# Performance work log

Measured on AMD Instinct MI355X. Metric: run time of the kernel, lower is better.

Reference implementation:

```python
import jax, jax.numpy as jnp
import numpy as np

B, S, E = 4, 2048, 1024
H = 16
D = E // H  # head_dim = 64


def setup_inputs() -> dict:
    key = jax.random.key(0)
    ks = jax.random.split(key, 7)
    query = jax.random.normal(ks[0], (B, S, E), dtype=jnp.float32)
    k_in = jax.random.normal(ks[1], (B, S, E), dtype=jnp.float32)
    v_in = jax.random.normal(ks[2], (B, S, E), dtype=jnp.float32)
    lim_qkv = 1.0 / np.sqrt(E)
    W_qkv = jax.random.uniform(ks[3], (E, 3 * E), jnp.float32, -lim_qkv, lim_qkv)
    b_qkv = jax.random.uniform(ks[4], (3 * E,), jnp.float32, -lim_qkv, lim_qkv)
    W_out = jax.random.uniform(ks[5], (E, E), jnp.float32, -lim_qkv, lim_qkv)
    b_out = jax.random.uniform(ks[6], (E,), jnp.float32, -lim_qkv, lim_qkv)
    return {"query": query, "key": k_in, "value": v_in,
            "W_qkv": W_qkv, "b_qkv": b_qkv, "W_out": W_out, "b_out": b_out}


def reference(query, key, value, W_qkv, b_qkv, W_out, b_out):
    # NOTE: original module ignores key/value; q,k,v all derived from query.
    b, s, e = query.shape
    qkv = query @ W_qkv + b_qkv                     # [B,S,3E]
    qkv = qkv.reshape(b, s, 3, H, D)
    q, k, v = qkv[:, :, 0], qkv[:, :, 1], qkv[:, :, 2]   # [B,S,H,D]
    scale = jnp.sqrt(jnp.asarray(D, dtype=jnp.float32))
    scores = jnp.einsum('bqhd,bkhd->bhqk', q, k) / scale  # [B,H,S,S]
    attn = jax.nn.softmax(scores, axis=-1)
    out = jnp.einsum('bhqk,bkhd->bqhd', attn, v).reshape(b, s, e)
    return out @ W_out + b_out
```

## Files before the change

kernel.cpp:

```cpp
#include <hip/hip_runtime.h>
#include <hip/hip_bf16.h>

#define Bc 4
#define Sc 2048
#define Ec 1024
#define Hc 16
#define Dc 64

typedef __bf16 bf16_t;
typedef __bf16 bf16x8 __attribute__((ext_vector_type(8)));
typedef float f32x4 __attribute__((ext_vector_type(4)));

extern "C" __device__ float __ocml_native_exp2_f32(float);

__device__ __forceinline__ f32x4 mfma16(bf16x8 a, bf16x8 b, f32x4 c) {
    return __builtin_amdgcn_mfma_f32_16x16x32_bf16(a, b, c, 0, 0, 0);
}

__device__ __forceinline__ void gload16(const bf16_t* g, bf16_t* l) {
    __builtin_amdgcn_global_load_lds(
        (const __attribute__((address_space(1))) unsigned int*)g,
        (__attribute__((address_space(3))) unsigned int*)l, 16, 0, 0);
}

__global__ __launch_bounds__(256)
void cvt_bf16(const float* __restrict__ in, bf16_t* __restrict__ out, int n4)
{
    int i = blockIdx.x * 256 + threadIdx.x;
    if (i >= n4) return;
    float4 v = ((const float4*)in)[i];
    alignas(8) bf16_t o[4];
    o[0] = (bf16_t)v.x; o[1] = (bf16_t)v.y; o[2] = (bf16_t)v.z; o[3] = (bf16_t)v.w;
    ((uint2*)out)[i] = *(uint2*)o;
}

__global__ __launch_bounds__(256)
void transpose_w(const float* __restrict__ W, bf16_t* __restrict__ Wt, int K, int N)
{
    __shared__ float T[64][65];
    const int kt = blockIdx.y, nt = blockIdx.x;
    const int r = threadIdx.x >> 4;
    const int c = (threadIdx.x & 15) * 4;
    #pragma unroll
    for (int p = 0; p < 4; p++) {
        float4 v = *(const float4*)(W + (size_t)(kt*64 + r + p*16)*N + nt*64 + c);
        T[r + p*16][c] = v.x; T[r + p*16][c+1] = v.y;
        T[r + p*16][c+2] = v.z; T[r + p*16][c+3] = v.w;
    }
    __syncthreads();
    #pragma unroll
    for (int p = 0; p < 4; p++) {
        int n = nt*64 + r + p*16;
        alignas(8) bf16_t tmp[4];
        #pragma unroll
        for (int j = 0; j < 4; j++) tmp[j] = (bf16_t)T[c + j][r + p*16];
        *(uint2*)(Wt + (size_t)n*K + kt*64 + c) = *(uint2*)tmp;
    }
}

__global__ __launch_bounds__(256)
void transpose_v(const bf16_t* __restrict__ qkv, bf16_t* __restrict__ vt)
{
    __shared__ bf16_t T[64][72];
    const int bh = blockIdx.y, st = blockIdx.x;
    const int b = bh >> 4, h = bh & 15;
    const int sr = threadIdx.x >> 3;
    const int dc = (threadIdx.x & 7) * 8;
    #pragma unroll
    for (int p = 0; p < 2; p++) {
        const bf16_t* src = qkv + (size_t)(b*Sc + st*64 + sr + p*32)*(3*Ec) + 2*Ec + h*Dc + dc;
        *(uint4*)&T[sr + p*32][dc] = *(const uint4*)src;
    }
    __syncthreads();
    const int dr = threadIdx.x >> 3;
    const int sc2 = (threadIdx.x & 7) * 8;
    #pragma unroll
    for (int p = 0; p < 2; p++) {
        alignas(16) bf16_t tmp[8];
        #pragma unroll
        for (int j = 0; j < 8; j++) {
            int q = sc2 + j;
            int o = ((q & 3) << 4) | (q >> 2);
            tmp[j] = T[o][dr + p*32];
        }
        *(uint4*)(vt + (size_t)bh*Dc*Sc + (size_t)(dr + p*32)*Sc + st*64 + sc2) = *(uint4*)tmp;
    }
}

template<int OUT_IS_F32>
__global__ __launch_bounds__(256)
void gemm_bt(const bf16_t* __restrict__ A, const bf16_t* __restrict__ Bt,
             const float* __restrict__ biasp, void* __restrict__ Cp,
             int M, int N, int K)
{
    __shared__ bf16_t As[128*32];
    __shared__ bf16_t Bs[128*32];

    const int tid  = threadIdx.x;
    const int wave = tid >> 6;
    const int lane = tid & 63;
    const int quad = lane >> 4;
    const int l16  = lane & 15;
    const int wm   = (wave >> 1) * 64;
    const int wn   = (wave & 1) * 64;
    const int m0   = blockIdx.y * 128;
    const int n0   = blockIdx.x * 128;

    const int srow = wave*32 + (lane >> 2);
    const int scol = (lane & 3) * 8;
    const bf16_t* ap0 = A  + (size_t)(m0 + srow)      * K + scol;
    const bf16_t* ap1 = A  + (size_t)(m0 + srow + 16) * K + scol;
    const bf16_t* bp0 = Bt + (size_t)(n0 + srow)      * K + scol;
    const bf16_t* bp1 = Bt + (size_t)(n0 + srow + 16) * K + scol;
    bf16_t* asl0 = &As[(wave*32)      * 32];
    bf16_t* asl1 = &As[(wave*32 + 16) * 32];
    bf16_t* bsl0 = &Bs[(wave*32)      * 32];
    bf16_t* bsl1 = &Bs[(wave*32 + 16) * 32];

    f32x4 acc[4][4] = {};

    for (int k0 = 0; k0 < K; k0 += 32) {
        gload16(ap0 + k0, asl0);
        gload16(ap1 + k0, asl1);
        gload16(bp0 + k0, bsl0);
        gload16(bp1 + k0, bsl1);
        __syncthreads();

        bf16x8 af[4], bfr[4];
        #pragma unroll
        for (int mi = 0; mi < 4; mi++)
            af[mi] = *(const bf16x8*)&As[(wm + mi*16 + l16)*32 + quad*8];
        #pragma unroll
        for (int ni = 0; ni < 4; ni++)
            bfr[ni] = *(const bf16x8*)&Bs[(wn + ni*16 + l16)*32 + quad*8];
        #pragma unroll
        for (int mi = 0; mi < 4; mi++)
            #pragma unroll
            for (int ni = 0; ni < 4; ni++)
                acc[mi][ni] = mfma16(af[mi], bfr[ni], acc[mi][ni]);
        __syncthreads();
    }

    float bv[4];
    #pragma unroll
    for (int ni = 0; ni < 4; ni++) bv[ni] = biasp[n0 + wn + ni*16 + l16];

    #pragma unroll
    for (int mi = 0; mi < 4; mi++)
        #pragma unroll
        for (int ni = 0; ni < 4; ni++)
            #pragma unroll
            for (int r = 0; r < 4; r++) {
                int row = m0 + wm + mi*16 + quad*4 + r;
                int col = n0 + wn + ni*16 + l16;
                float v = acc[mi][ni][r] + bv[ni];
                if (OUT_IS_F32) ((float*)Cp)[(size_t)row * N + col] = v;
                else            ((bf16_t*)Cp)[(size_t)row * N + col] = (bf16_t)v;
            }
}

__global__ __launch_bounds__(256, 4)
void attn4(const bf16_t* __restrict__ qkv, const bf16_t* __restrict__ vt,
           bf16_t* __restrict__ aout)
{
    __shared__ bf16_t Ks[64][72];
    __shared__ bf16_t Vs[64][72];
    __shared__ bf16_t Ps[4][32][72];

    const int tid  = threadIdx.x;
    const int wave = tid >> 6;
    const int lane = tid & 63;
    const int quad = lane >> 4;
    const int l16  = lane & 15;
    const int bh   = blockIdx.y;
    const int b    = bh >> 4;
    const int h    = bh & 15;
    const int qt   = blockIdx.x;
    const float kscale = 0.125f * 1.44269504088896340736f;

    bf16x8 qf[2][2];
    #pragma unroll
    for (int mi = 0; mi < 2; mi++) {
        const bf16_t* qrow = qkv + (size_t)(b*Sc + qt*128 + wave*32 + mi*16 + l16)*(3*Ec) + h*Dc;
        qf[mi][0] = *(const bf16x8*)(qrow + quad*8);
        qf[mi][1] = *(const bf16x8*)(qrow + 32 + quad*8);
        #pragma unroll
        for (int f = 0; f < 2; f++)
            #pragma unroll
            for (int e = 0; e < 8; e++)
                qf[mi][f][e] = (bf16_t)((float)qf[mi][f][e] * kscale);
    }

    bf16x8 ones;
    #pragma unroll
    for (int e = 0; e < 8; e++) ones[e] = (bf16_t)1.0f;

    f32x4 acc[2][4] = {};
    f32x4 acc_l[2] = {};

    const int krw   = tid >> 2;
    const int dbase = (tid & 3) * 16;

    const bf16_t* kbase = qkv + (size_t)(b*Sc + krw)*(3*Ec) + Ec + h*Dc + dbase;
    const bf16_t* vbase = vt + (size_t)bh*Dc*Sc + (size_t)krw*Sc + dbase;
    const size_t kstep = (size_t)64 * (3*Ec);
    uint4 ku0 = ((const uint4*)kbase)[0];
    uint4 ku1 = ((const uint4*)kbase)[1];
    uint4 vu0 = ((const uint4*)vbase)[0];
    uint4 vu1 = ((const uint4*)vbase)[1];

    for (int kt = 0; kt < Sc/64; kt++) {
        __syncthreads();
        *(uint4*)&Ks[krw][dbase]     = ku0;
        *(uint4*)&Ks[krw][dbase + 8] = ku1;
        *(uint4*)&Vs[krw][dbase]     = vu0;
        *(uint4*)&Vs[krw][dbase + 8] = vu1;
        __syncthreads();

        if (kt < Sc/64 - 1) {
            const bf16_t* kn = kbase + (size_t)(kt+1) * kstep;
            const bf16_t* vn = vbase + (kt+1) * 64;
            ku0 = ((const uint4*)kn)[0];
            ku1 = ((const uint4*)kn)[1];
            vu0 = ((const uint4*)vn)[0];
            vu1 = ((const uint4*)vn)[1];
        }

        bf16x8 kf[4][2];
        #pragma unroll
        for (int ni = 0; ni < 4; ni++) {
            kf[ni][0] = *(const bf16x8*)&Ks[ni*16 + l16][quad*8];
            kf[ni][1] = *(const bf16x8*)&Ks[ni*16 + l16][32 + quad*8];
        }

        #pragma unroll
        for (int mi = 0; mi < 2; mi++) {
            f32x4 sf[4];
            #pragma unroll
            for (int ni = 0; ni < 4; ni++) {
                f32x4 z = {};
                z = mfma16(qf[mi][0], kf[ni][0], z);
                z = mfma16(qf[mi][1], kf[ni][1], z);
                sf[ni] = z;
            }
            #pragma unroll
            for (int rr = 0; rr < 4; rr++) {
                float p0 = __ocml_native_exp2_f32(sf[0][rr]);
                float p1 = __ocml_native_exp2_f32(sf[1][rr]);
                float p2 = __ocml_native_exp2_f32(sf[2][rr]);
                float p3 = __ocml_native_exp2_f32(sf[3][rr]);
                alignas(8) bf16_t pw[4];
                pw[0] = (bf16_t)p0; pw[1] = (bf16_t)p1;
                pw[2] = (bf16_t)p2; pw[3] = (bf16_t)p3;
                *(uint2*)&Ps[wave][mi*16 + quad*4 + rr][4*l16] = *(uint2*)pw;
            }
        }

        asm volatile("s_waitcnt lgkmcnt(0)" ::: "memory");

        bf16x8 pf[2][2];
        #pragma unroll
        for (int mi = 0; mi < 2; mi++) {
            pf[mi][0] = *(const bf16x8*)&Ps[wave][mi*16 + l16][quad*8];
            pf[mi][1] = *(const bf16x8*)&Ps[wave][mi*16 + l16][32 + quad*8];
        }
        #pragma unroll
        for (int mi = 0; mi < 2; mi++) {
            acc_l[mi] = mfma16(pf[mi][0], ones, acc_l[mi]);
            acc_l[mi] = mfma16(pf[mi][1], ones, acc_l[mi]);
        }
        #pragma unroll
        for (int ni = 0; ni < 4; ni++) {
            bf16x8 v0 = *(const bf16x8*)&Vs[ni*16 + l16][quad*8];
            bf16x8 v1 = *(const bf16x8*)&Vs[ni*16 + l16][32 + quad*8];
            #pragma unroll
            for (int mi = 0; mi < 2; mi++) {
                acc[mi][ni] = mfma16(pf[mi][0], v0, acc[mi][ni]);
                acc[mi][ni] = mfma16(pf[mi][1], v1, acc[mi][ni]);
            }
        }
    }

    #pragma unroll
    for (int mi = 0; mi < 2; mi++)
        #pragma unroll
        for (int rr = 0; rr < 4; rr++) {
            float inv = 1.0f / acc_l[mi][rr];
            int row = qt*128 + wave*32 + mi*16 + quad*4 + rr;
            #pragma unroll
            for (int ni = 0; ni < 4; ni++) {
                int col = h*Dc + ni*16 + l16;
                aout[(size_t)(b*Sc + row)*Ec + col] = (bf16_t)(acc[mi][ni][rr] * inv);
            }
        }
}

extern "C" void kernel_launch(void* const* d_in, const int* in_sizes, int n_in,
                              void* d_out, int out_size, void* d_ws, size_t ws_size,
                              hipStream_t stream) {
    const float* query = (const float*)d_in[0];
    const float* W_qkv = (const float*)d_in[3];
    const float* b_qkv = (const float*)d_in[4];
    const float* W_out = (const float*)d_in[5];
    const float* b_out = (const float*)d_in[6];
    float* out = (float*)d_out;

    const size_t MT = (size_t)Bc * Sc;
    char* ws = (char*)d_ws;
    bf16_t* qbf     = (bf16_t*)ws;
    bf16_t* qkv_ws  = (bf16_t*)(ws + MT*Ec*2);
    bf16_t* vt_ws   = (bf16_t*)(ws + MT*Ec*2 + MT*3*Ec*2);
    bf16_t* wqkv_t  = (bf16_t*)(ws + MT*Ec*2 + MT*3*Ec*2 + MT*Ec*2);
    bf16_t* wout_t  = (bf16_t*)(ws + MT*Ec*2 + MT*3*Ec*2 + MT*Ec*2 + (size_t)3*Ec*Ec*2);

    cvt_bf16<<<(MT*Ec/4 + 255)/256, 256, 0, stream>>>(query, qbf, (int)(MT*Ec/4));
    transpose_w<<<dim3(3*Ec/64, Ec/64), 256, 0, stream>>>(W_qkv, wqkv_t, Ec, 3*Ec);
    transpose_w<<<dim3(Ec/64, Ec/64), 256, 0, stream>>>(W_out, wout_t, Ec, Ec);

    gemm_bt<0><<<dim3(3*Ec/128, MT/128), 256, 0, stream>>>(
        qbf, wqkv_t, b_qkv, qkv_ws, (int)MT, 3*Ec, Ec);

    transpose_v<<<dim3(Sc/64, Bc*Hc), 256, 0, stream>>>(qkv_ws, vt_ws);

    attn4<<<dim3(Sc/128, Bc*Hc), 256, 0, stream>>>(qkv_ws, vt_ws, qbf);

    gemm_bt<1><<<dim3(Ec/128, MT/128), 256, 0, stream>>>(
        qbf, wout_t, b_out, out, (int)MT, Ec, Ec);
}
```

Before: 344.1 us.

## Double GEMM K-step per barrier and enlarge attention query tile to 256 rows

The GEMM now loads two 32-wide K slices per iteration into separate LDS buffers, which halves the number of barriers per K sweep. The attention kernel processes 64 query rows per wave (256 per block) instead of 32, so each K/V tile loaded into LDS is reused across twice as many queries. The cost is higher register and LDS use: the launch bound drops to 2 blocks per SM, and the attention grid is halved to 512 blocks, which may hurt latency hiding.

```diff
diff --git a/kernel.cpp b/kernel.cpp
--- a/kernel.cpp
+++ b/kernel.cpp
@@ -93,8 +93,8 @@
              const float* __restrict__ biasp, void* __restrict__ Cp,
              int M, int N, int K)
 {
-    __shared__ bf16_t As[128*32];
-    __shared__ bf16_t Bs[128*32];
+    __shared__ bf16_t As[2][128*32];
+    __shared__ bf16_t Bs[2][128*32];
 
     const int tid  = threadIdx.x;
     const int wave = tid >> 6;
@@ -112,32 +112,43 @@
     const bf16_t* ap1 = A  + (size_t)(m0 + srow + 16) * K + scol;
     const bf16_t* bp0 = Bt + (size_t)(n0 + srow)      * K + scol;
     const bf16_t* bp1 = Bt + (size_t)(n0 + srow + 16) * K + scol;
-    bf16_t* asl0 = &As[(wave*32)      * 32];
-    bf16_t* asl1 = &As[(wave*32 + 16) * 32];
-    bf16_t* bsl0 = &Bs[(wave*32)      * 32];
-    bf16_t* bsl1 = &Bs[(wave*32 + 16) * 32];
+    bf16_t* asl0 = &As[0][(wave*32)      * 32];
+    bf16_t* asl1 = &As[0][(wave*32 + 16) * 32];
+    bf16_t* bsl0 = &Bs[0][(wave*32)      * 32];
+    bf16_t* bsl1 = &Bs[0][(wave*32 + 16) * 32];
+    bf16_t* asl2 = &As[1][(wave*32)      * 32];
+    bf16_t* asl3 = &As[1][(wave*32 + 16) * 32];
+    bf16_t* bsl2 = &Bs[1][(wave*32)      * 32];
+    bf16_t* bsl3 = &Bs[1][(wave*32 + 16) * 32];
 
     f32x4 acc[4][4] = {};
 
-    for (int k0 = 0; k0 < K; k0 += 32) {
-        gload16(ap0 + k0, asl0);
-        gload16(ap1 + k0, asl1);
-        gload16(bp0 + k0, bsl0);
-        gload16(bp1 + k0, bsl1);
+    for (int k0 = 0; k0 < K; k0 += 64) {
+        gload16(ap0 + k0,      asl0);
+        gload16(ap1 + k0,      asl1);
+        gload16(ap0 + k0 + 32, asl2);
+        gload16(ap1 + k0 + 32, asl3);
+        gload16(bp0 + k0,      bsl0);
+        gload16(bp1 + k0,      bsl1);
+        gload16(bp0 + k0 + 32, bsl2);
+        gload16(bp1 + k0 + 32, bsl3);
         __syncthreads();
 
-        bf16x8 af[4], bfr[4];
-        #pragma unroll
-        for (int mi = 0; mi < 4; mi++)
-            af[mi] = *(const bf16x8*)&As[(wm + mi*16 + l16)*32 + quad*8];
-        #pragma unroll
-        for (int ni = 0; ni < 4; ni++)
-            bfr[ni] = *(const bf16x8*)&Bs[(wn + ni*16 + l16)*32 + quad*8];
-        #pragma unroll
-        for (int mi = 0; mi < 4; mi++)
+        #pragma unroll
+        for (int kc = 0; kc < 2; kc++) {
+            bf16x8 af[4], bfr[4];
+            #pragma unroll
+            for (int mi = 0; mi < 4; mi++)
+                af[mi] = *(const bf16x8*)&As[kc][(wm + mi*16 + l16)*32 + quad*8];
             #pragma unroll
             for (int ni = 0; ni < 4; ni++)
-                acc[mi][ni] = mfma16(af[mi], bfr[ni], acc[mi][ni]);
+                bfr[ni] = *(const bf16x8*)&Bs[kc][(wn + ni*16 + l16)*32 + quad*8];
+            #pragma unroll
+            for (int mi = 0; mi < 4; mi++)
+                #pragma unroll
+                for (int ni = 0; ni < 4; ni++)
+                    acc[mi][ni] = mfma16(af[mi], bfr[ni], acc[mi][ni]);
+        }
         __syncthreads();
     }
 
@@ -159,13 +170,13 @@
             }
 }
 
-__global__ __launch_bounds__(256, 4)
-void attn4(const bf16_t* __restrict__ qkv, const bf16_t* __restrict__ vt,
+__global__ __launch_bounds__(256, 2)
+void attn5(const bf16_t* __restrict__ qkv, const bf16_t* __restrict__ vt,
            bf16_t* __restrict__ aout)
 {
     __shared__ bf16_t Ks[64][72];
     __shared__ bf16_t Vs[64][72];
-    __shared__ bf16_t Ps[4][32][72];
+    __shared__ bf16_t Ps[4][64][72];
 
     const int tid  = threadIdx.x;
     const int wave = tid >> 6;
@@ -178,10 +189,10 @@
     const int qt   = blockIdx.x;
     const float kscale = 0.125f * 1.44269504088896340736f;
 
-    bf16x8 qf[2][2];
-    #pragma unroll
-    for (int mi = 0; mi < 2; mi++) {
-        const bf16_t* qrow = qkv + (size_t)(b*Sc + qt*128 + wave*32 + mi*16 + l16)*(3*Ec) + h*Dc;
+    bf16x8 qf[4][2];
+    #pragma unroll
+    for (int mi = 0; mi < 4; mi++) {
+        const bf16_t* qrow = qkv + (size_t)(b*Sc + qt*256 + wave*64 + mi*16 + l16)*(3*Ec) + h*Dc;
         qf[mi][0] = *(const bf16x8*)(qrow + quad*8);
         qf[mi][1] = *(const bf16x8*)(qrow + 32 + quad*8);
         #pragma unroll
@@ -195,8 +206,8 @@
     #pragma unroll
     for (int e = 0; e < 8; e++) ones[e] = (bf16_t)1.0f;
 
-    f32x4 acc[2][4] = {};
-    f32x4 acc_l[2] = {};
+    f32x4 acc[4][4] = {};
+    f32x4 acc_l[4] = {};
 
     const int krw   = tid >> 2;
     const int dbase = (tid & 3) * 16;
@@ -234,7 +245,7 @@
         }
 
         #pragma unroll
-        for (int mi = 0; mi < 2; mi++) {
+        for (int mi = 0; mi < 4; mi++) {
             f32x4 sf[4];
             #pragma unroll
             for (int ni = 0; ni < 4; ni++) {
@@ -258,14 +269,14 @@
 
         asm volatile("s_waitcnt lgkmcnt(0)" ::: "memory");
 
-        bf16x8 pf[2][2];
-        #pragma unroll
-        for (int mi = 0; mi < 2; mi++) {
+        bf16x8 pf[4][2];
+        #pragma unroll
+        for (int mi = 0; mi < 4; mi++) {
             pf[mi][0] = *(const bf16x8*)&Ps[wave][mi*16 + l16][quad*8];
             pf[mi][1] = *(const bf16x8*)&Ps[wave][mi*16 + l16][32 + quad*8];
         }
         #pragma unroll
-        for (int mi = 0; mi < 2; mi++) {
+        for (int mi = 0; mi < 4; mi++) {
             acc_l[mi] = mfma16(pf[mi][0], ones, acc_l[mi]);
             acc_l[mi] = mfma16(pf[mi][1], ones, acc_l[mi]);
         }
@@ -274,7 +285,7 @@
             bf16x8 v0 = *(const bf16x8*)&Vs[ni*16 + l16][quad*8];
             bf16x8 v1 = *(const bf16x8*)&Vs[ni*16 + l16][32 + quad*8];
             #pragma unroll
-            for (int mi = 0; mi < 2; mi++) {
+            for (int mi = 0; mi < 4; mi++) {
                 acc[mi][ni] = mfma16(pf[mi][0], v0, acc[mi][ni]);
                 acc[mi][ni] = mfma16(pf[mi][1], v1, acc[mi][ni]);
             }
@@ -282,11 +293,11 @@
     }
 
     #pragma unroll
-    for (int mi = 0; mi < 2; mi++)
+    for (int mi = 0; mi < 4; mi++)
         #pragma unroll
         for (int rr = 0; rr < 4; rr++) {
             float inv = 1.0f / acc_l[mi][rr];
-            int row = qt*128 + wave*32 + mi*16 + quad*4 + rr;
+            int row = qt*256 + wave*64 + mi*16 + quad*4 + rr;
             #pragma unroll
             for (int ni = 0; ni < 4; ni++) {
                 int col = h*Dc + ni*16 + l16;
@@ -322,7 +333,7 @@
 
     transpose_v<<<dim3(Sc/64, Bc*Hc), 256, 0, stream>>>(qkv_ws, vt_ws);
 
-    attn4<<<dim3(Sc/128, Bc*Hc), 256, 0, stream>>>(qkv_ws, vt_ws, qbf);
+    attn5<<<dim3(Sc/256, Bc*Hc), 256, 0, stream>>>(qkv_ws, vt_ws, qbf);
 
     gemm_bt<1><<<dim3(Ec/128, MT/128), 256, 0, stream>>>(
         qbf, wout_t, b_out, out, (int)MT, Ec, Ec);
```

Result: faster. 321.4 us (-6.6%).
